# Kernel optimization log

Measured on AMD Instinct MI355X. Metric: run time of the kernel, lower is better.

Reference implementation:

```python
import jax, jax.numpy as jnp
import numpy as np

B, S, I, H, O = 64, 512, 1024, 1024, 1024


def setup_inputs() -> dict:
    key = jax.random.key(0)
    ks = jax.random.split(key, 10)
    s = 0.02
    return {
        "x": jax.random.normal(ks[0], (B, S, I), dtype=jnp.float32),
        "W_hi": jax.random.normal(ks[1], (H, H), dtype=jnp.float32) * s,
        "W_ii": jax.random.normal(ks[2], (I, H), dtype=jnp.float32) * s,
        "W_hf": jax.random.normal(ks[3], (H, H), dtype=jnp.float32) * s,
        "W_if": jax.random.normal(ks[4], (I, H), dtype=jnp.float32) * s,
        "W_ho": jax.random.normal(ks[5], (H, H), dtype=jnp.float32) * s,
        "W_io": jax.random.normal(ks[6], (I, H), dtype=jnp.float32) * s,
        "W_hg": jax.random.normal(ks[7], (H, H), dtype=jnp.float32) * s,
        "W_ig": jax.random.normal(ks[8], (I, H), dtype=jnp.float32) * s,
        "W_y": jax.random.normal(ks[9], (H, O), dtype=jnp.float32) * s,
    }


def reference(x, W_hi, W_ii, W_hf, W_if, W_ho, W_io, W_hg, W_ig, W_y):
    b = x.shape[0]
    h0 = jnp.zeros((b, W_hi.shape[0]), dtype=x.dtype)
    c0 = jnp.zeros_like(h0)

    def step(carry, x_t):
        h, c = carry
        i = jax.nn.sigmoid(h @ W_hi + x_t @ W_ii)
        f = jax.nn.sigmoid(h @ W_hf + x_t @ W_if)
        o = jax.nn.sigmoid(h @ W_ho + x_t @ W_io)
        g = jnp.tanh(h @ W_hg + x_t @ W_ig)
        c = f * c + i * g
        h = o * jnp.tanh(c)
        return (h, c), None

    # scan over time: x -> [S, B, I]
    (h_T, _), _ = jax.lax.scan(step, (h0, c0), jnp.swapaxes(x, 0, 1))
    return h_T @ W_y
```

## Files before the change

### kernel.cpp

```cpp
#include <hip/hip_runtime.h>


typedef __bf16 bfv8 __attribute__((ext_vector_type(8)));
typedef float f32x4 __attribute__((ext_vector_type(4)));
typedef unsigned int u32v4 __attribute__((ext_vector_type(4)));

__device__ __forceinline__ unsigned short f2bf(float x) {
    union { float f; unsigned int u; } v; v.f = x;
    unsigned int r = (v.u + 0x7FFFu + ((v.u >> 16) & 1u)) >> 16;
    return (unsigned short)r;
}
__device__ __forceinline__ float bf2f(unsigned short s) {
    union { unsigned int u; float f; } v; v.u = ((unsigned int)s) << 16;
    return v.f;
}

struct SrcPtrs { const float* p[9]; };

#define ISSUE8(A, P, O0, O1, O2, O3, O4, O5, O6, O7)                         \
    asm volatile(                                                            \
        "global_load_dwordx4 %0, %8, off offset:" O0 " sc0 sc1\n\t"          \
        "global_load_dwordx4 %1, %8, off offset:" O1 " sc0 sc1\n\t"          \
        "global_load_dwordx4 %2, %8, off offset:" O2 " sc0 sc1\n\t"          \
        "global_load_dwordx4 %3, %8, off offset:" O3 " sc0 sc1\n\t"          \
        "global_load_dwordx4 %4, %8, off offset:" O4 " sc0 sc1\n\t"          \
        "global_load_dwordx4 %5, %8, off offset:" O5 " sc0 sc1\n\t"          \
        "global_load_dwordx4 %6, %8, off offset:" O6 " sc0 sc1\n\t"          \
        "global_load_dwordx4 %7, %8, off offset:" O7 " sc0 sc1"              \
        : "=&v"(A[0]), "=&v"(A[1]), "=&v"(A[2]), "=&v"(A[3]),                \
          "=&v"(A[4]), "=&v"(A[5]), "=&v"(A[6]), "=&v"(A[7])                 \
        : "v"(P)                                                             \
        : "memory")

#define ISSUE8C(A, P, O0, O1, O2, O3, O4, O5, O6, O7)                        \
    asm volatile(                                                            \
        "global_load_dwordx4 %0, %8, off offset:" O0 "\n\t"                  \
        "global_load_dwordx4 %1, %8, off offset:" O1 "\n\t"                  \
        "global_load_dwordx4 %2, %8, off offset:" O2 "\n\t"                  \
        "global_load_dwordx4 %3, %8, off offset:" O3 "\n\t"                  \
        "global_load_dwordx4 %4, %8, off offset:" O4 "\n\t"                  \
        "global_load_dwordx4 %5, %8, off offset:" O5 "\n\t"                  \
        "global_load_dwordx4 %6, %8, off offset:" O6 "\n\t"                  \
        "global_load_dwordx4 %7, %8, off offset:" O7                         \
        : "=&v"(A[0]), "=&v"(A[1]), "=&v"(A[2]), "=&v"(A[3]),                \
          "=&v"(A[4]), "=&v"(A[5]), "=&v"(A[6]), "=&v"(A[7])                 \
        : "v"(P)                                                             \
        : "memory")

#define WAIT8(N, A)                                                          \
    do {                                                                     \
        asm volatile("s_waitcnt vmcnt(" N ")"                                \
                     : "+v"(A[0]), "+v"(A[1]), "+v"(A[2]), "+v"(A[3]),       \
                       "+v"(A[4]), "+v"(A[5]), "+v"(A[6]), "+v"(A[7])        \
                     :: "memory");                                           \
        __builtin_amdgcn_sched_barrier(0);                                   \
    } while (0)

#define CONSUME8(A, IT0)                                                     \
    _Pragma("unroll")                                                        \
    for (int j = 0; j < 8; ++j) {                                            \
        _Pragma("unroll")                                                    \
        for (int n = 0; n < 2; ++n) {                                        \
            const int off = (((((IT0) + j) << 1) | n) << 10) + (lane << 4);  \
            acc[n] = __builtin_amdgcn_mfma_f32_16x16x32_bf16(                \
                A[j], *(const bfv8*)(Lw + off), acc[n], 0, 0, 0);            \
        }                                                                    \
    }

__global__ __launch_bounds__(256) void pack_weights(SrcPtrs sp,
                                                    unsigned short* __restrict__ Whp,
                                                    unsigned short* __restrict__ Wip,
                                                    unsigned short* __restrict__ Wy) {
    __shared__ float tile[64][65];
    const int z = blockIdx.z;
    const float* __restrict__ src = sp.p[z];
    const int n0 = blockIdx.x * 64, k0 = blockIdx.y * 64;
    const int tc = threadIdx.x & 63, tq = threadIdx.x >> 6;

    #pragma unroll
    for (int r = 0; r < 16; ++r) {
        const int kk = tq * 16 + r;
        tile[kk][tc] = src[(size_t)(k0 + kk) * 1024 + n0 + tc];
    }
    __syncthreads();
    #pragma unroll
    for (int r = 0; r < 16; ++r) {
        const int nl = tq * 16 + r;
        const int n = n0 + nl;
        const int k = k0 + tc;
        const unsigned short v = f2bf(tile[tc][nl]);
        if (z < 8) {
            const int g = z & 3;
            const int blk = n >> 3;
            const int c = (g << 3) | (n & 7);
            const int lanef = (c & 15) | (((k >> 3) & 3) << 4);
            const size_t off = ((size_t)((((blk << 5) | (k >> 5)) << 1) | (c >> 4)) << 9)
                             + (lanef << 3) + (k & 7);
            (z < 4 ? Whp : Wip)[off] = v;
        } else {
            Wy[(size_t)n * 1024 + k] = v;
        }
    }
}

__global__ __launch_bounds__(256) void convert_x(const float* __restrict__ x,
                                                 unsigned short* __restrict__ xT) {
    const size_t gid = (size_t)blockIdx.x * 256 + threadIdx.x;
    const int i0 = (int)(gid & 255) * 4;
    const size_t row = gid >> 8;
    const int t = (int)(row >> 6), b = (int)(row & 63);
    const float4 v = *reinterpret_cast<const float4*>(x + (((size_t)b * 512 + t) << 10) + i0);
    ushort4 o;
    o.x = f2bf(v.x); o.y = f2bf(v.y); o.z = f2bf(v.z); o.w = f2bf(v.w);
    *reinterpret_cast<ushort4*>(xT + (row << 10) + i0) = o;
}

__global__ __launch_bounds__(256) void lstm_pc(const unsigned short* __restrict__ xT,
                                               const unsigned short* __restrict__ Whp,
                                               const unsigned short* __restrict__ Wip,
                                               unsigned short* __restrict__ hlo,
                                               int* __restrict__ flg,
                                               int* __restrict__ xflg,
                                               unsigned short* __restrict__ ring) {
    __shared__ struct {
        __align__(16) unsigned char wp[65536];
        __align__(16) unsigned char pad[32768];
        __align__(16) unsigned short hs[64][8];
        int sig;
        int Lrdy[4];
    } L;
    unsigned char* Lw = L.wp;

    const int tid = threadIdx.x;
    const int w = tid >> 6;
    const int lane = tid & 63;
    const int lr = lane & 15;
    const int kq = lane >> 4;
    const bool isFactory = (blockIdx.x >= 128);
    const int b = isFactory ? (blockIdx.x - 128) : blockIdx.x;

    {
        const unsigned short* src = (isFactory ? Wip : Whp) + ((size_t)b << 15);
        #pragma unroll
        for (int s = 0; s < 16; ++s) {
            const int c = s * 256 + tid;
            *(bfv8*)(L.wp + c * 16) = *(const bfv8*)(src + c * 8);
        }
    }
    if (tid == 0) L.sig = 0;
    if (tid < 4) L.Lrdy[tid] = 0;
    __syncthreads();

    const int roff = ((w << 4) + lr) * 1024 + kq * 8;

    if (isFactory) {
        for (int tt = 0; tt < 512; ++tt) {
            if (tt >= 4) {
                const int* cf = flg + (b << 9);
                while (__hip_atomic_load(cf, __ATOMIC_RELAXED, __HIP_MEMORY_SCOPE_AGENT) < tt - 3)
                    __builtin_amdgcn_s_sleep(2);
            }
            const unsigned short* Axp = xT + ((size_t)tt << 16) + roff;
            f32x4 acc[2] = {};
            bfv8 a0[8], a1[8];
            ISSUE8(a0, Axp, "0", "64", "128", "192", "256", "320", "384", "448");
            ISSUE8(a1, Axp, "512", "576", "640", "704", "768", "832", "896", "960");
            WAIT8("8", a0);
            CONSUME8(a0, 0);
            ISSUE8(a0, Axp, "1024", "1088", "1152", "1216", "1280", "1344", "1408", "1472");
            WAIT8("8", a1);
            CONSUME8(a1, 8);
            ISSUE8(a1, Axp, "1536", "1600", "1664", "1728", "1792", "1856", "1920", "1984");
            WAIT8("8", a0);
            CONSUME8(a0, 16);
            WAIT8("0", a1);
            CONSUME8(a1, 24);

            unsigned short vv[8];
            #pragma unroll
            for (int n = 0; n < 2; ++n)
                #pragma unroll
                for (int r = 0; r < 4; ++r)
                    vv[n * 4 + r] = f2bf(acc[n][r]);
            unsigned short* rp = ring + (((size_t)(b << 2) + (tt & 3)) * 4 + w) * 512 + lane * 8;
            asm volatile("global_store_dwordx4 %0, %1, off sc0 sc1"
                         :: "v"(rp), "v"(*(const u32v4*)vv) : "memory");
            asm volatile("s_waitcnt vmcnt(0)" ::: "memory");
            if (lane == 0) {
                const int old = atomicAdd(&L.sig, 1);
                if (old == 4 * tt + 3)
                    asm volatile("global_store_dword %0, %1, off sc0 sc1"
                                 :: "v"(xflg + (b << 9)), "v"(tt + 1) : "memory");
            }
        }
        return;
    }

    float cst[4] = {0.f, 0.f, 0.f, 0.f};
    const int mw = w;

    for (int t = 0; t < 512; ++t) {
        const unsigned short* __restrict__ hin =
            (t < 10) ? (hlo + ((size_t)t << 16))
                     : (xT + ((size_t)(t - 10) << 16));
        unsigned short* __restrict__ hout =
            (t + 1 < 10) ? (hlo + ((size_t)(t + 1) << 16))
                         : (const_cast<unsigned short*>(xT) + ((size_t)(t + 1 - 10) << 16));

        const int* xfp = xflg + (b << 9);
        while (__hip_atomic_load(xfp, __ATOMIC_RELAXED, __HIP_MEMORY_SCOPE_AGENT) < t + 1)
            __builtin_amdgcn_s_sleep(1);
        u32v4 xp;
        {
            const unsigned short* rp =
                ring + (((size_t)(b << 2) + (t & 3)) * 4 + mw) * 512 + lane * 8;
            asm volatile("global_load_dwordx4 %0, %1, off sc0 sc1"
                         : "=v"(xp) : "v"(rp) : "memory");
        }

        if (t > 0) {
            const int* fp = flg + (((mw << 5) + (lane & 31)) << 9);
            for (;;) {
                const int f = __hip_atomic_load(fp, __ATOMIC_RELAXED,
                                                __HIP_MEMORY_SCOPE_AGENT);
                if (__all(f >= t)) break;
                __builtin_amdgcn_s_sleep(1);
            }
            __hip_atomic_store(&L.Lrdy[mw], t, __ATOMIC_RELAXED,
                               __HIP_MEMORY_SCOPE_WORKGROUP);
        }
        auto ldswait = [&](int g) {
            if (t == 0) return;
            while (__hip_atomic_load(&L.Lrdy[g], __ATOMIC_RELAXED,
                                     __HIP_MEMORY_SCOPE_WORKGROUP) < t) { }
            asm volatile("" ::: "memory");
        };

        const unsigned short* hp = hin + roff;
        f32x4 acc[2] = {};
        bfv8 a0[8], a1[8];
        ldswait(0);
        ISSUE8C(a0, hp, "0", "64", "128", "192", "256", "320", "384", "448");
        ldswait(1);
        ISSUE8C(a1, hp, "512", "576", "640", "704", "768", "832", "896", "960");
        WAIT8("8", a0);
        CONSUME8(a0, 0);
        ldswait(2);
        ISSUE8C(a0, hp, "1024", "1088", "1152", "1216", "1280", "1344", "1408", "1472");
        WAIT8("8", a1);
        CONSUME8(a1, 8);
        ldswait(3);
        ISSUE8C(a1, hp, "1536", "1600", "1664", "1728", "1792", "1856", "1920", "1984");
        WAIT8("8", a0);
        CONSUME8(a0, 16);
        WAIT8("0", a1);
        CONSUME8(a1, 24);

        asm volatile("s_waitcnt vmcnt(0)" : "+v"(xp) :: "memory");
        __builtin_amdgcn_sched_barrier(0);
        {
            const unsigned short* xs = (const unsigned short*)&xp;
            #pragma unroll
            for (int n = 0; n < 2; ++n)
                #pragma unroll
                for (int r = 0; r < 4; ++r)
                    acc[n][r] += bf2f(xs[n * 4 + r]);
        }

        const bool low = (lr & 8) == 0;
        unsigned short hsv[4];
        #pragma unroll
        for (int r = 0; r < 4; ++r) {
            const float s0 = acc[0][r], s1 = acc[1][r];
            const float x0 = __shfl_xor(s0, 8);
            const float x1 = __shfl_xor(s1, 8);
            const float pi = low ? s0 : x0;
            const float pf = low ? x0 : s0;
            const float po = low ? s1 : x1;
            const float pg = low ? x1 : s1;
            const float ig = 1.f / (1.f + __expf(-pi));
            const float fg = 1.f / (1.f + __expf(-pf));
            const float og = 1.f / (1.f + __expf(-po));
            const float gg = 1.f - 2.f / (__expf(2.f * pg) + 1.f);
            const float cn = fg * cst[r] + ig * gg;
            cst[r] = cn;
            hsv[r] = f2bf(og * (1.f - 2.f / (__expf(2.f * cn) + 1.f)));
        }

        if (low) {
            #pragma unroll
            for (int r = 0; r < 4; ++r)
                L.hs[(mw << 4) + (kq << 2) + r][lr] = hsv[r];
        }
        asm volatile("s_waitcnt lgkmcnt(0)" ::: "memory");
        __builtin_amdgcn_sched_barrier(0);
        if (lane < 16) {
            const int row = (mw << 4) + lane;
            const u32v4 hv = *reinterpret_cast<const u32v4*>(&L.hs[row][0]);
            asm volatile("global_store_dwordx4 %0, %1, off sc0 sc1 nt"
                         :: "v"(hout + (size_t)row * 1024 + (b << 3)), "v"(hv)
                         : "memory");
        }
        asm volatile("s_waitcnt vmcnt(0)" ::: "memory");
        if (lane == 0) {
            const int old = atomicAdd(&L.sig, 1);
            if (old == 4 * t + 3)
                asm volatile("global_store_dword %0, %1, off sc0 sc1"
                             :: "v"(flg + (b << 9)), "v"(t + 1) : "memory");
        }
    }
}

__global__ __launch_bounds__(256) void final_gemm(const unsigned short* __restrict__ h_in,
                                                  const unsigned short* __restrict__ WyT,
                                                  float* __restrict__ out) {
    const int tid = threadIdx.x;
    const int w = tid >> 6;
    const int lane = tid & 63;
    const int lr = lane & 15;
    const int kq = lane >> 4;
    const int c0 = blockIdx.x * 16;
    const int k0 = w * 256;

    f32x4 acc[4] = {};
    #pragma unroll 2
    for (int it = 0; it < 8; ++it) {
        const int k = k0 + it * 32 + kq * 8;
        const bfv8 bfr = *reinterpret_cast<const bfv8*>(WyT + (size_t)(c0 + lr) * 1024 + k);
        #pragma unroll
        for (int m = 0; m < 4; ++m) {
            const bfv8 a = *reinterpret_cast<const bfv8*>(h_in + (size_t)(m * 16 + lr) * 1024 + k);
            acc[m] = __builtin_amdgcn_mfma_f32_16x16x32_bf16(a, bfr, acc[m], 0, 0, 0);
        }
    }
    __shared__ float red[4][64][17];
    #pragma unroll
    for (int m = 0; m < 4; ++m)
        #pragma unroll
        for (int r = 0; r < 4; ++r)
            red[w][m * 16 + kq * 4 + r][lr] = acc[m][r];
    __syncthreads();
    #pragma unroll
    for (int u = 0; u < 4; ++u) {
        const int item = u * 256 + tid;
        const int b = item >> 4;
        const int jr = item & 15;
        const float s = red[0][b][jr] + red[1][b][jr] + red[2][b][jr] + red[3][b][jr];
        out[b * 1024 + c0 + jr] = s;
    }
}

extern "C" void kernel_launch(void* const* d_in, const int* in_sizes, int n_in,
                              void* d_out, int out_size, void* d_ws, size_t ws_size,
                              hipStream_t stream) {
    const float* x = (const float*)d_in[0];
    SrcPtrs sp;
    sp.p[0] = (const float*)d_in[1];
    sp.p[1] = (const float*)d_in[3];
    sp.p[2] = (const float*)d_in[5];
    sp.p[3] = (const float*)d_in[7];
    sp.p[4] = (const float*)d_in[2];
    sp.p[5] = (const float*)d_in[4];
    sp.p[6] = (const float*)d_in[6];
    sp.p[7] = (const float*)d_in[8];
    sp.p[8] = (const float*)d_in[9];

    char* ws = (char*)d_ws;
    unsigned short* Whp  = (unsigned short*)(ws + 0);
    unsigned short* Wip  = (unsigned short*)(ws + 8388608);
    unsigned short* Wy   = (unsigned short*)(ws + 16777216);
    unsigned short* xT   = (unsigned short*)(ws + 18874368);
    unsigned short* hlo  = (unsigned short*)(ws + 85983232);
    int*            flg  = (int*)(ws + 87293952);
    int*            xflg = (int*)(ws + 87556096);
    unsigned short* ring = (unsigned short*)(ws + 87818240);

    pack_weights<<<dim3(16, 16, 9), 256, 0, stream>>>(sp, Whp, Wip, Wy);
    convert_x<<<32768, 256, 0, stream>>>(x, xT);
    hipMemsetAsync(hlo, 0, 131072, stream);
    hipMemsetAsync(flg, 0, 262144, stream);
    hipMemsetAsync(xflg, 0, 262144, stream);

    lstm_pc<<<256, 256, 0, stream>>>(xT, Whp, Wip, hlo, flg, xflg, ring);

    final_gemm<<<64, 256, 0, stream>>>(xT + ((size_t)502 << 16), Wy, (float*)d_out);
}
```

Before: 3.704 ms.

## Replace flag-based h sync with sentinel-poisoned ring buffer polling

```diff
diff --git a/kernel.cpp b/kernel.cpp
--- a/kernel.cpp
+++ b/kernel.cpp
@@ -32,21 +32,6 @@
         : "v"(P)                                                             \
         : "memory")
 
-#define ISSUE8C(A, P, O0, O1, O2, O3, O4, O5, O6, O7)                        \
-    asm volatile(                                                            \
-        "global_load_dwordx4 %0, %8, off offset:" O0 "\n\t"                  \
-        "global_load_dwordx4 %1, %8, off offset:" O1 "\n\t"                  \
-        "global_load_dwordx4 %2, %8, off offset:" O2 "\n\t"                  \
-        "global_load_dwordx4 %3, %8, off offset:" O3 "\n\t"                  \
-        "global_load_dwordx4 %4, %8, off offset:" O4 "\n\t"                  \
-        "global_load_dwordx4 %5, %8, off offset:" O5 "\n\t"                  \
-        "global_load_dwordx4 %6, %8, off offset:" O6 "\n\t"                  \
-        "global_load_dwordx4 %7, %8, off offset:" O7                         \
-        : "=&v"(A[0]), "=&v"(A[1]), "=&v"(A[2]), "=&v"(A[3]),                \
-          "=&v"(A[4]), "=&v"(A[5]), "=&v"(A[6]), "=&v"(A[7])                 \
-        : "v"(P)                                                             \
-        : "memory")
-
 #define WAIT8(N, A)                                                          \
     do {                                                                     \
         asm volatile("s_waitcnt vmcnt(" N ")"                                \
@@ -65,6 +50,24 @@
             acc[n] = __builtin_amdgcn_mfma_f32_16x16x32_bf16(                \
                 A[j], *(const bfv8*)(Lw + off), acc[n], 0, 0, 0);            \
         }                                                                    \
+    }
+
+#define ISSUE32(P)                                                           \
+    do {                                                                     \
+        ISSUE8(A0, P, "0", "64", "128", "192", "256", "320", "384", "448");  \
+        ISSUE8(A1, P, "512", "576", "640", "704", "768", "832", "896", "960"); \
+        ISSUE8(A2, P, "1024", "1088", "1152", "1216", "1280", "1344", "1408", "1472"); \
+        ISSUE8(A3, P, "1536", "1600", "1664", "1728", "1792", "1856", "1920", "1984"); \
+    } while (0)
+
+#define CHKMAX(A)                                                            \
+    _Pragma("unroll")                                                        \
+    for (int j = 0; j < 8; ++j) {                                            \
+        const u32v4 u = __builtin_bit_cast(u32v4, A[j]);                     \
+        mh = mh > u.x ? mh : u.x;                                            \
+        mh = mh > u.y ? mh : u.y;                                            \
+        mh = mh > u.z ? mh : u.z;                                            \
+        mh = mh > u.w ? mh : u.w;                                            \
     }
 
 __global__ __launch_bounds__(256) void pack_weights(SrcPtrs sp,
@@ -118,16 +121,14 @@
 __global__ __launch_bounds__(256) void lstm_pc(const unsigned short* __restrict__ xT,
                                                const unsigned short* __restrict__ Whp,
                                                const unsigned short* __restrict__ Wip,
-                                               unsigned short* __restrict__ hlo,
-                                               int* __restrict__ flg,
+                                               unsigned short* __restrict__ hring,
                                                int* __restrict__ xflg,
+                                               int* __restrict__ cflg,
                                                unsigned short* __restrict__ ring) {
     __shared__ struct {
         __align__(16) unsigned char wp[65536];
         __align__(16) unsigned char pad[32768];
         __align__(16) unsigned short hs[64][8];
-        int sig;
-        int Lrdy[4];
     } L;
     unsigned char* Lw = L.wp;
 
@@ -147,34 +148,32 @@
             *(bfv8*)(L.wp + c * 16) = *(const bfv8*)(src + c * 8);
         }
     }
-    if (tid == 0) L.sig = 0;
-    if (tid < 4) L.Lrdy[tid] = 0;
     __syncthreads();
 
     const int roff = ((w << 4) + lr) * 1024 + kq * 8;
+    const int pw = (b << 2) + w;
 
     if (isFactory) {
         for (int tt = 0; tt < 512; ++tt) {
-            if (tt >= 4) {
-                const int* cf = flg + (b << 9);
-                while (__hip_atomic_load(cf, __ATOMIC_RELAXED, __HIP_MEMORY_SCOPE_AGENT) < tt - 3)
-                    __builtin_amdgcn_s_sleep(2);
-            }
+            const int* cfp = cflg + pw * 32;
+            while (__hip_atomic_load(cfp, __ATOMIC_RELAXED, __HIP_MEMORY_SCOPE_AGENT) < tt - 4)
+                __builtin_amdgcn_s_sleep(2);
+
             const unsigned short* Axp = xT + ((size_t)tt << 16) + roff;
             f32x4 acc[2] = {};
-            bfv8 a0[8], a1[8];
-            ISSUE8(a0, Axp, "0", "64", "128", "192", "256", "320", "384", "448");
-            ISSUE8(a1, Axp, "512", "576", "640", "704", "768", "832", "896", "960");
-            WAIT8("8", a0);
-            CONSUME8(a0, 0);
-            ISSUE8(a0, Axp, "1024", "1088", "1152", "1216", "1280", "1344", "1408", "1472");
-            WAIT8("8", a1);
-            CONSUME8(a1, 8);
-            ISSUE8(a1, Axp, "1536", "1600", "1664", "1728", "1792", "1856", "1920", "1984");
-            WAIT8("8", a0);
-            CONSUME8(a0, 16);
-            WAIT8("0", a1);
-            CONSUME8(a1, 24);
+            bfv8 A0[8], A1[8];
+            ISSUE8(A0, Axp, "0", "64", "128", "192", "256", "320", "384", "448");
+            ISSUE8(A1, Axp, "512", "576", "640", "704", "768", "832", "896", "960");
+            WAIT8("8", A0);
+            CONSUME8(A0, 0);
+            ISSUE8(A0, Axp, "1024", "1088", "1152", "1216", "1280", "1344", "1408", "1472");
+            WAIT8("8", A1);
+            CONSUME8(A1, 8);
+            ISSUE8(A1, Axp, "1536", "1600", "1664", "1728", "1792", "1856", "1920", "1984");
+            WAIT8("8", A0);
+            CONSUME8(A0, 16);
+            WAIT8("0", A1);
+            CONSUME8(A1, 24);
 
             unsigned short vv[8];
             #pragma unroll
@@ -186,85 +185,71 @@
             asm volatile("global_store_dwordx4 %0, %1, off sc0 sc1"
                          :: "v"(rp), "v"(*(const u32v4*)vv) : "memory");
             asm volatile("s_waitcnt vmcnt(0)" ::: "memory");
-            if (lane == 0) {
-                const int old = atomicAdd(&L.sig, 1);
-                if (old == 4 * tt + 3)
-                    asm volatile("global_store_dword %0, %1, off sc0 sc1"
-                                 :: "v"(xflg + (b << 9)), "v"(tt + 1) : "memory");
-            }
+            if (lane == 0)
+                asm volatile("global_store_dword %0, %1, off sc0 sc1"
+                             :: "v"(xflg + pw * 32), "v"(tt + 1) : "memory");
         }
         return;
     }
 
     float cst[4] = {0.f, 0.f, 0.f, 0.f};
-    const int mw = w;
+    bfv8 A0[8], A1[8], A2[8], A3[8];
+    const u32v4 PZ = {0xFFFFFFFFu, 0xFFFFFFFFu, 0xFFFFFFFFu, 0xFFFFFFFFu};
+
+    {
+        const unsigned short* hp = hring + roff;
+        ISSUE32(hp);
+    }
 
     for (int t = 0; t < 512; ++t) {
-        const unsigned short* __restrict__ hin =
-            (t < 10) ? (hlo + ((size_t)t << 16))
-                     : (xT + ((size_t)(t - 10) << 16));
-        unsigned short* __restrict__ hout =
-            (t + 1 < 10) ? (hlo + ((size_t)(t + 1) << 16))
-                         : (const_cast<unsigned short*>(xT) + ((size_t)(t + 1 - 10) << 16));
-
-        const int* xfp = xflg + (b << 9);
+        const unsigned short* hp = hring + ((size_t)(t & 15) << 16) + roff;
+
+        const int* xfp = xflg + pw * 32;
         while (__hip_atomic_load(xfp, __ATOMIC_RELAXED, __HIP_MEMORY_SCOPE_AGENT) < t + 1)
             __builtin_amdgcn_s_sleep(1);
         u32v4 xp;
+        const unsigned short* rp = ring + (((size_t)(b << 2) + (t & 3)) * 4 + w) * 512 + lane * 8;
+        asm volatile("global_load_dwordx4 %0, %1, off sc0 sc1"
+                     : "=v"(xp) : "v"(rp) : "memory");
+
+        int guard = 0;
+        for (;;) {
+            WAIT8("0", A0); WAIT8("0", A1); WAIT8("0", A2); WAIT8("0", A3);
+            asm volatile("s_waitcnt vmcnt(0)" : "+v"(xp) :: "memory");
+            __builtin_amdgcn_sched_barrier(0);
+            unsigned mh = 0;
+            CHKMAX(A0) CHKMAX(A1) CHKMAX(A2) CHKMAX(A3)
+            if (!__any(mh == 0xFFFFFFFFu) || ++guard > 65536) break;
+            ISSUE32(hp);
+        }
+
+        if (lane == 0)
+            asm volatile("global_store_dword %0, %1, off sc0 sc1"
+                         :: "v"(cflg + pw * 32), "v"(t) : "memory");
+
+        if (t >= 1 && lane < 16) {
+            unsigned short* pz = hring + ((size_t)((t - 1) & 15) << 16)
+                               + (size_t)w * 16384 + (size_t)b * 128;
+            asm volatile("global_store_dwordx4 %0, %1, off sc0 sc1"
+                         :: "v"(pz + lane * 8), "v"(PZ) : "memory");
+        }
+
+        f32x4 acc[2] = {};
+        CONSUME8(A0, 0);
+        CONSUME8(A1, 8);
+        CONSUME8(A2, 16);
+        CONSUME8(A3, 24);
+
         {
-            const unsigned short* rp =
-                ring + (((size_t)(b << 2) + (t & 3)) * 4 + mw) * 512 + lane * 8;
-            asm volatile("global_load_dwordx4 %0, %1, off sc0 sc1"
-                         : "=v"(xp) : "v"(rp) : "memory");
-        }
-
-        if (t > 0) {
-            const int* fp = flg + (((mw << 5) + (lane & 31)) << 9);
-            for (;;) {
-                const int f = __hip_atomic_load(fp, __ATOMIC_RELAXED,
-                                                __HIP_MEMORY_SCOPE_AGENT);
-                if (__all(f >= t)) break;
-                __builtin_amdgcn_s_sleep(1);
-            }
-            __hip_atomic_store(&L.Lrdy[mw], t, __ATOMIC_RELAXED,
-                               __HIP_MEMORY_SCOPE_WORKGROUP);
-        }
-        auto ldswait = [&](int g) {
-            if (t == 0) return;
-            while (__hip_atomic_load(&L.Lrdy[g], __ATOMIC_RELAXED,
-                                     __HIP_MEMORY_SCOPE_WORKGROUP) < t) { }
-            asm volatile("" ::: "memory");
-        };
-
-        const unsigned short* hp = hin + roff;
-        f32x4 acc[2] = {};
-        bfv8 a0[8], a1[8];
-        ldswait(0);
-        ISSUE8C(a0, hp, "0", "64", "128", "192", "256", "320", "384", "448");
-        ldswait(1);
-        ISSUE8C(a1, hp, "512", "576", "640", "704", "768", "832", "896", "960");
-        WAIT8("8", a0);
-        CONSUME8(a0, 0);
-        ldswait(2);
-        ISSUE8C(a0, hp, "1024", "1088", "1152", "1216", "1280", "1344", "1408", "1472");
-        WAIT8("8", a1);
-        CONSUME8(a1, 8);
-        ldswait(3);
-        ISSUE8C(a1, hp, "1536", "1600", "1664", "1728", "1792", "1856", "1920", "1984");
-        WAIT8("8", a0);
-        CONSUME8(a0, 16);
-        WAIT8("0", a1);
-        CONSUME8(a1, 24);
-
-        asm volatile("s_waitcnt vmcnt(0)" : "+v"(xp) :: "memory");
-        __builtin_amdgcn_sched_barrier(0);
-        {
-            const unsigned short* xs = (const unsigned short*)&xp;
-            #pragma unroll
-            for (int n = 0; n < 2; ++n)
-                #pragma unroll
-                for (int r = 0; r < 4; ++r)
-                    acc[n][r] += bf2f(xs[n * 4 + r]);
+            const unsigned d0 = xp.x, d1 = xp.y, d2 = xp.z, d3 = xp.w;
+            acc[0][0] += bf2f((unsigned short)(d0 & 0xFFFFu));
+            acc[0][1] += bf2f((unsigned short)(d0 >> 16));
+            acc[0][2] += bf2f((unsigned short)(d1 & 0xFFFFu));
+            acc[0][3] += bf2f((unsigned short)(d1 >> 16));
+            acc[1][0] += bf2f((unsigned short)(d2 & 0xFFFFu));
+            acc[1][1] += bf2f((unsigned short)(d2 >> 16));
+            acc[1][2] += bf2f((unsigned short)(d3 & 0xFFFFu));
+            acc[1][3] += bf2f((unsigned short)(d3 >> 16));
         }
 
         const bool low = (lr & 8) == 0;
@@ -290,23 +275,23 @@
         if (low) {
             #pragma unroll
             for (int r = 0; r < 4; ++r)
-                L.hs[(mw << 4) + (kq << 2) + r][lr] = hsv[r];
+                L.hs[(w << 4) + (kq << 2) + r][lr] = hsv[r];
         }
         asm volatile("s_waitcnt lgkmcnt(0)" ::: "memory");
         __builtin_amdgcn_sched_barrier(0);
-        if (lane < 16) {
-            const int row = (mw << 4) + lane;
-            const u32v4 hv = *reinterpret_cast<const u32v4*>(&L.hs[row][0]);
-            asm volatile("global_store_dwordx4 %0, %1, off sc0 sc1 nt"
-                         :: "v"(hout + (size_t)row * 1024 + (b << 3)), "v"(hv)
-                         : "memory");
-        }
-        asm volatile("s_waitcnt vmcnt(0)" ::: "memory");
-        if (lane == 0) {
-            const int old = atomicAdd(&L.sig, 1);
-            if (old == 4 * t + 3)
-                asm volatile("global_store_dword %0, %1, off sc0 sc1"
-                             :: "v"(flg + (b << 9)), "v"(t + 1) : "memory");
+        {
+            unsigned short* hout = hring + ((size_t)((t + 1) & 15) << 16);
+            if (lane < 16) {
+                const int row = (w << 4) + lane;
+                const u32v4 hv = *reinterpret_cast<const u32v4*>(&L.hs[row][0]);
+                asm volatile("global_store_dwordx4 %0, %1, off sc0 sc1"
+                             :: "v"(hout + (size_t)row * 1024 + (b << 3)), "v"(hv)
+                             : "memory");
+            }
+        }
+        if (t < 511) {
+            const unsigned short* hn = hring + ((size_t)((t + 1) & 15) << 16) + roff;
+            ISSUE32(hn);
         }
     }
 }
@@ -366,22 +351,23 @@
     sp.p[8] = (const float*)d_in[9];
 
     char* ws = (char*)d_ws;
-    unsigned short* Whp  = (unsigned short*)(ws + 0);
-    unsigned short* Wip  = (unsigned short*)(ws + 8388608);
-    unsigned short* Wy   = (unsigned short*)(ws + 16777216);
-    unsigned short* xT   = (unsigned short*)(ws + 18874368);
-    unsigned short* hlo  = (unsigned short*)(ws + 85983232);
-    int*            flg  = (int*)(ws + 87293952);
-    int*            xflg = (int*)(ws + 87556096);
-    unsigned short* ring = (unsigned short*)(ws + 87818240);
+    unsigned short* Whp   = (unsigned short*)(ws + 0);
+    unsigned short* Wip   = (unsigned short*)(ws + 8388608);
+    unsigned short* Wy    = (unsigned short*)(ws + 16777216);
+    unsigned short* xT    = (unsigned short*)(ws + 18874368);
+    unsigned short* hring = (unsigned short*)(ws + 85983232);
+    unsigned short* ring  = (unsigned short*)(ws + 88080384);
+    int*            xflg  = (int*)(ws + 90177536);
+    int*            cflg  = (int*)(ws + 90243072);
 
     pack_weights<<<dim3(16, 16, 9), 256, 0, stream>>>(sp, Whp, Wip, Wy);
     convert_x<<<32768, 256, 0, stream>>>(x, xT);
-    hipMemsetAsync(hlo, 0, 131072, stream);
-    hipMemsetAsync(flg, 0, 262144, stream);
-    hipMemsetAsync(xflg, 0, 262144, stream);
-
-    lstm_pc<<<256, 256, 0, stream>>>(xT, Whp, Wip, hlo, flg, xflg, ring);
-
-    final_gemm<<<64, 256, 0, stream>>>(xT + ((size_t)502 << 16), Wy, (float*)d_out);
-}
+    hipMemsetAsync(hring, 0xFF, 16 * 131072, stream);
+    hipMemsetAsync(hring, 0x00, 131072, stream);
+    hipMemsetAsync(xflg, 0x00, 65536, stream);
+    hipMemsetAsync(cflg, 0xFF, 65536, stream);
+
+    lstm_pc<<<256, 256, 0, stream>>>(xT, Whp, Wip, hring, xflg, cflg, ring);
+
+    final_gemm<<<64, 256, 0, stream>>>(hring, Wy, (float*)d_out);
+}
```

Measured after the change: 6.295 ms. 70.0% more time.
